# Optimization experiments

Hardware: AMD Instinct MI355X
Metric: run time of the kernel (lower is better)

The kernel has to match this reference:

```python
import jax, jax.numpy as jnp
import numpy as np

NUM_GRAPHS = 1024  # number of graphs in the batch (readout segments)


def setup_inputs() -> dict:
    key = jax.random.key(0)
    ks = jax.random.split(key, 10)
    N, F_IN, F1, F2, E = 100000, 64, 128, 64, 3200000
    x = jax.random.normal(ks[0], (N, F_IN), dtype=jnp.float32)
    adj = jax.random.randint(ks[1], (2, E), 0, N, dtype=jnp.int64)
    batch = jnp.sort(jax.random.randint(ks[2], (N,), 0, NUM_GRAPHS, dtype=jnp.int64))
    def xavier(k, shape):
        fan_in, fan_out = shape
        lim = jnp.sqrt(6.0 / (fan_in + fan_out))
        return jax.random.uniform(k, shape, jnp.float32, -lim, lim)
    W1 = xavier(ks[3], (F_IN, F1)); b1 = jax.random.uniform(ks[4], (F1,), jnp.float32)
    W2 = xavier(ks[5], (F1, F2));  b2 = jax.random.uniform(ks[6], (F2,), jnp.float32)
    Wm = xavier(ks[7], (2 * F2, F2)); bm = jax.random.uniform(ks[8], (F2,), jnp.float32)
    return {"x": x, "adj": adj, "batch": batch,
            "W1": W1, "b1": b1, "W2": W2, "b2": b2, "Wm": Wm, "bm": bm}


def _gcn_conv(x, W, b, src, dst):
    # GCNConv: out = D^{-1/2} (A + I) D^{-1/2} X W + b
    N = x.shape[0]
    h = x @ W  # [N, F_out]
    loops = jnp.arange(N, dtype=src.dtype)
    src_a = jnp.concatenate([src, loops])  # add self-loops
    dst_a = jnp.concatenate([dst, loops])
    deg = jax.ops.segment_sum(jnp.ones(src_a.shape[0], h.dtype), dst_a, num_segments=N)
    dinv = jax.lax.rsqrt(deg)  # deg >= 1 due to self-loops
    norm = dinv[src_a] * dinv[dst_a]  # [E+N]
    msg = h[src_a] * norm[:, None]    # gather + scale (memory-bound)
    return jax.ops.segment_sum(msg, dst_a, num_segments=N) + b


def _readout_meanmax(x, batch):
    G = NUM_GRAPHS
    s = jax.ops.segment_sum(x, batch, num_segments=G)
    cnt = jax.ops.segment_sum(jnp.ones(x.shape[0], x.dtype), batch, num_segments=G)
    mean = s / jnp.maximum(cnt, 1.0)[:, None]
    mx = jax.ops.segment_max(x, batch, num_segments=G)
    return jnp.concatenate([mean, mx], axis=1)  # [G, 2*F2]


def reference(x, adj, batch, W1, b1, W2, b2, Wm, bm):
    src, dst = adj[0], adj[1]
    h = jax.nn.relu(_gcn_conv(x, W1, b1, src, dst))
    h = _gcn_conv(h, W2, b2, src, dst)
    r = _readout_meanmax(h, batch)
    return r @ Wm + bm
```

## Files before the change

### kernel.cpp

```cpp
#include <hip/hip_runtime.h>
#include <hip/hip_fp16.h>
#include <cstdint>
#include <cstddef>

#define NGRAPH 1024
#define CHUNK 8192
#define SCTHREADS 512
#define SCIT (CHUNK / SCTHREADS)
#define MAXB 512
#define CAP 16384

typedef _Float16 f16x8 __attribute__((ext_vector_type(8)));
typedef float f32x4 __attribute__((ext_vector_type(4)));
typedef float f32x2 __attribute__((ext_vector_type(2)));


__global__ __launch_bounds__(SCTHREADS) void scatter1_kernel(const int* __restrict__ src,
        const int* __restrict__ dst, int E, int B,
        int* __restrict__ bcnt, unsigned* __restrict__ ebuck) {
    __shared__ unsigned sorted[CHUNK];
    __shared__ int h[MAXB];
    __shared__ int lo[MAXB];
    __shared__ int cur[MAXB];
    __shared__ int gbase[MAXB];
    int blk = blockIdx.x, tid = threadIdx.x;
    int base = blk * CHUNK;
    int cnt_i = E - base; if (cnt_i > CHUNK) cnt_i = CHUNK;

    h[tid] = 0;
    __syncthreads();

    unsigned rd[SCIT], rs[SCIT];
    #pragma unroll
    for (int it = 0; it < SCIT; ++it) {
        int i = base + tid + it * SCTHREADS;
        if (i < E) {
            rd[it] = (unsigned)dst[i];
            rs[it] = (unsigned)src[i];
            atomicAdd(&h[rd[it] >> 8], 1);
        } else rd[it] = 0xFFFFFFFFu;
    }
    __syncthreads();

    int hv = h[tid];
    if (tid < B) gbase[tid] = hv ? atomicAdd(&bcnt[tid], hv) : 0;

    for (int o = 1; o < SCTHREADS; o <<= 1) {
        int t = (tid >= o) ? h[tid - o] : 0;
        __syncthreads();
        h[tid] += t;
        __syncthreads();
    }
    int excl = h[tid] - hv;
    lo[tid] = excl;
    cur[tid] = excl;
    __syncthreads();

    #pragma unroll
    for (int it = 0; it < SCIT; ++it) {
        if (rd[it] != 0xFFFFFFFFu) {
            int b = rd[it] >> 8;
            int p = atomicAdd(&cur[b], 1);
            sorted[p] = ((rd[it] & 255u) << 24) | rs[it];
        }
    }
    __syncthreads();

    for (int j = tid; j < cnt_i; j += SCTHREADS) {
        int l = (int)(((long long)j * B) / cnt_i);
        if (l > B - 1) l = B - 1;
        while (lo[l] > j) --l;
        while (l + 1 < B && lo[l + 1] <= j) ++l;
        ebuck[(size_t)l * CAP + gbase[l] + (j - lo[l])] = sorted[j];
    }
}

__global__ __launch_bounds__(256) void fine_kernel(const unsigned* __restrict__ ebuck,
        const int* __restrict__ bcnt, const float* __restrict__ x, int N, int B,
        int* __restrict__ row_beg, int* __restrict__ row_end, float* __restrict__ dinv,
        int* __restrict__ esrc, unsigned char* __restrict__ xs) {
    __shared__ int hcnt[256];
    __shared__ int sc[256];
    __shared__ int loff[256];
    __shared__ float sdinv[256];
    int b = blockIdx.x, tid = threadIdx.x;
    int beg = b * CAP;
    int cnt = bcnt[b];
    hcnt[tid] = 0;
    __syncthreads();
    for (int e = tid; e < cnt; e += 256)
        atomicAdd(&hcnt[ebuck[beg + e] >> 24], 1);
    __syncthreads();
    int v = hcnt[tid];
    int n = (b << 8) + tid;
    int vp = (v + 15) & ~15;
    if (vp < 48) vp = 48;
    if (n >= N) vp = 0;
    sc[tid] = vp; __syncthreads();
    for (int o = 1; o < 256; o <<= 1) {
        int t = (tid >= o) ? sc[tid - o] : 0;
        __syncthreads();
        sc[tid] += t;
        __syncthreads();
    }
    int excl = sc[tid] - vp;
    float d = rsqrtf((float)(v + 1));
    if (n < N) {
        row_beg[n] = beg + excl;
        row_end[n] = beg + excl + vp;
        dinv[n] = d;
    }
    loff[tid] = excl;
    sdinv[tid] = d;
    __syncthreads();
    for (int e = tid; e < cnt; e += 256) {
        unsigned u = ebuck[beg + e];
        int p = atomicAdd(&loff[u >> 24], 1);
        esrc[beg + p] = (int)(u & 0xFFFFFF);
    }
    for (int p = excl + v; p < excl + vp; ++p) esrc[beg + p] = N;
    const float4* xr = (const float4*)x;
    #pragma unroll
    for (int it = 0; it < 16; ++it) {
        int j = tid + it * 256;
        int node = j >> 4, cc = j & 15;
        int gn = (b << 8) + node;
        if (gn < N) {
            float dd = sdinv[node];
            float4 vv = xr[(size_t)gn * 16 + cc];
            int lo2 = __builtin_amdgcn_cvt_pk_fp8_f32(vv.x * dd, vv.y * dd, 0, false);
            int hi2 = __builtin_amdgcn_cvt_pk_fp8_f32(vv.z * dd, vv.w * dd, 0, false);
            ((unsigned*)xs)[(size_t)gn * 16 + cc] =
                (unsigned)(lo2 & 0xffff) | ((unsigned)(hi2 & 0xffff) << 16);
        }
    }
}

__global__ __launch_bounds__(256) void prep_kernel(const float* __restrict__ W1,
        const float* __restrict__ W2, __half* __restrict__ W1s, __half* __restrict__ W2s,
        const int* __restrict__ batch, int N, int* __restrict__ goff,
        int* __restrict__ bcnt, unsigned char* __restrict__ xsq,
        unsigned char* __restrict__ tsq, float* __restrict__ zbias) {
    int t = threadIdx.x;
    if (blockIdx.x == 0) {
        #pragma unroll
        for (int it = 0; it < 4; ++it) {
            int s = t + it * 256;
            int n = s & 15, q = (s >> 4) & 3, nt = (s >> 6) & 7, ks = s >> 9;
            int k0 = ks * 32 + q * 8, col = nt * 16 + n;
            __align__(16) __half h[8];
            #pragma unroll
            for (int j = 0; j < 8; ++j) h[j] = (__half)W1[(k0 + j) * 128 + col];
            *((uint4*)&W1s[(size_t)s * 8]) = *(uint4*)h;
        }
        #pragma unroll
        for (int it = 0; it < 4; ++it) {
            int s = t + it * 256;
            int n = s & 15, q = (s >> 4) & 3, n2 = (s >> 6) & 3, ks2 = s >> 8;
            int k0 = ks2 * 32 + q * 8, col = n2 * 16 + n;
            __align__(16) __half h[8];
            #pragma unroll
            for (int j = 0; j < 8; ++j) h[j] = (__half)W2[(k0 + j) * 64 + col];
            *((uint4*)&W2s[(size_t)s * 8]) = *(uint4*)h;
        }
        uint4 z; z.x = 0; z.y = 0; z.z = 0; z.w = 0;
        if (t < 4)
            ((uint4*)(xsq + (size_t)N * 64))[t] = z;
        if (t < 4)
            ((uint4*)(tsq + (size_t)N * 64))[t] = z;
        if (t < 64) zbias[t] = 0.f;
    } else {
        int g = (blockIdx.x - 1) * 256 + t;
        if (g < MAXB) bcnt[g] = 0;
        if (g > NGRAPH) return;
        if (g == NGRAPH) { goff[g] = N; return; }
        int lo = 0, hi = N;
        while (lo < hi) {
            int mid = (lo + hi) >> 1;
            if (batch[mid] < g) lo = mid + 1; else hi = mid;
        }
        goff[g] = lo;
    }
}

__device__ __forceinline__ void acc8q(f32x2* a, const uint2& u) {
    a[0] += __builtin_amdgcn_cvt_pk_f32_fp8(u.x, false);
    a[1] += __builtin_amdgcn_cvt_pk_f32_fp8(u.x, true);
    a[2] += __builtin_amdgcn_cvt_pk_f32_fp8(u.y, false);
    a[3] += __builtin_amdgcn_cvt_pk_f32_fp8(u.y, true);
}

__device__ __forceinline__ void agg_core_q(const uint2* __restrict__ ts2,
        const int* __restrict__ esrc, int beg, int endp, int n, int g, int c,
        float* a) {
    f32x2 h0[4] = {}, h1[4] = {};
    if (g == 0) acc8q(h0, ts2[(size_t)n * 8 + c]);
    int U = (endp - beg) >> 3;
    int e = beg + g;
    if (U == 6) {
        int i0 = esrc[e], i1 = esrc[e + 8], i2 = esrc[e + 16];
        int i3 = esrc[e + 24], i4 = esrc[e + 32], i5 = esrc[e + 40];
        uint2 u0 = ts2[(size_t)i0 * 8 + c];
        uint2 u1 = ts2[(size_t)i1 * 8 + c];
        uint2 u2 = ts2[(size_t)i2 * 8 + c];
        uint2 u3 = ts2[(size_t)i3 * 8 + c];
        uint2 u4 = ts2[(size_t)i4 * 8 + c];
        uint2 u5 = ts2[(size_t)i5 * 8 + c];
        acc8q(h0, u0); acc8q(h1, u1); acc8q(h0, u2); acc8q(h1, u3);
        acc8q(h0, u4); acc8q(h1, u5);
    } else if (U > 0) {
        int i0 = esrc[e], i1 = esrc[e + 8];
        for (int t = (U >> 1) - 1; t > 0; --t) {
            int j0 = esrc[e + 16], j1 = esrc[e + 24];
            acc8q(h0, ts2[(size_t)i0 * 8 + c]);
            acc8q(h1, ts2[(size_t)i1 * 8 + c]);
            i0 = j0; i1 = j1; e += 16;
        }
        acc8q(h0, ts2[(size_t)i0 * 8 + c]);
        acc8q(h1, ts2[(size_t)i1 * 8 + c]);
    }
    #pragma unroll
    for (int i = 0; i < 4; ++i) {
        a[2 * i]     = h0[i].x + h1[i].x;
        a[2 * i + 1] = h0[i].y + h1[i].y;
    }
}

__global__ __launch_bounds__(256) void agg_q2h_kernel(const unsigned char* __restrict__ ts,
        const int* __restrict__ esrc, const int* __restrict__ row_beg,
        const int* __restrict__ row_end, const float* __restrict__ dinv,
        const float* __restrict__ bias, __half* __restrict__ out, int N) {
    int n = blockIdx.x * 4 + (threadIdx.x >> 6);
    if (n >= N) return;
    int lane = threadIdx.x & 63;
    int g = lane >> 3, c = lane & 7;
    const uint2* ts2 = (const uint2*)ts;
    float a[8];
    agg_core_q(ts2, esrc, row_beg[n], row_end[n], n, g, c, a);
    #pragma unroll
    for (int i = 0; i < 8; ++i) {
        a[i] += __shfl_xor(a[i], 8, 64);
        a[i] += __shfl_xor(a[i], 16, 64);
        a[i] += __shfl_xor(a[i], 32, 64);
    }
    if (g == 0) {
        float d = dinv[n];
        float4 bb0 = ((const float4*)bias)[c * 2];
        float4 bb1 = ((const float4*)bias)[c * 2 + 1];
        __align__(16) __half2 h[4];
        h[0] = __floats2half2_rn(a[0] * d + bb0.x, a[1] * d + bb0.y);
        h[1] = __floats2half2_rn(a[2] * d + bb0.z, a[3] * d + bb0.w);
        h[2] = __floats2half2_rn(a[4] * d + bb1.x, a[5] * d + bb1.y);
        h[3] = __floats2half2_rn(a[6] * d + bb1.z, a[7] * d + bb1.w);
        ((uint4*)out)[(size_t)n * 8 + c] = *(uint4*)h;
    }
}

__global__ __launch_bounds__(256) void fusedmlp_kernel(const __half* __restrict__ A,
        const __half* __restrict__ W1s, const __half* __restrict__ W2s,
        const float* __restrict__ b1, const float* __restrict__ dinv,
        unsigned char* __restrict__ T, int N) {
    __shared__ __align__(16) __half h1t[4][16][136];
    int tid = threadIdx.x;
    int w = tid >> 6, lane = tid & 63;
    int n15 = lane & 15, q = lane >> 4;
    int base = blockIdx.x * 64 + w * 16;

    int m = base + n15; if (m >= N) m = N - 1;
    const uint4* Ar = (const uint4*)(A + (size_t)m * 64);
    uint4 ua0 = Ar[q];
    uint4 ua1 = Ar[4 + q];
    f16x8 a10 = *(f16x8*)&ua0;
    f16x8 a11 = *(f16x8*)&ua1;
    const uint4* W1f = (const uint4*)W1s;
    #pragma unroll
    for (int nt = 0; nt < 8; ++nt) {
        f32x4 c = {0.f, 0.f, 0.f, 0.f};
        uint4 ub0 = W1f[(nt * 4 + q) * 16 + n15];
        uint4 ub1 = W1f[((8 + nt) * 4 + q) * 16 + n15];
        c = __builtin_amdgcn_mfma_f32_16x16x32_f16(a10, *(f16x8*)&ub0, c, 0, 0, 0);
        c = __builtin_amdgcn_mfma_f32_16x16x32_f16(a11, *(f16x8*)&ub1, c, 0, 0, 0);
        float bv = b1[nt * 16 + n15];
        #pragma unroll
        for (int rr = 0; rr < 4; ++rr) {
            float hv = fmaxf(c[rr] + bv, 0.f);
            h1t[w][q * 4 + rr][nt * 16 + n15] = (__half)hv;
        }
    }
    __syncthreads();

    f16x8 a2[4];
    #pragma unroll
    for (int ks2 = 0; ks2 < 4; ++ks2)
        a2[ks2] = *(f16x8*)&h1t[w][n15][ks2 * 32 + q * 8];
    const uint4* W2f = (const uint4*)W2s;
    #pragma unroll
    for (int n2 = 0; n2 < 4; ++n2) {
        f32x4 c = {0.f, 0.f, 0.f, 0.f};
        #pragma unroll
        for (int ks2 = 0; ks2 < 4; ++ks2) {
            uint4 ub = W2f[((ks2 * 4 + n2) * 4 + q) * 16 + n15];
            c = __builtin_amdgcn_mfma_f32_16x16x32_f16(a2[ks2], *(f16x8*)&ub, c, 0, 0, 0);
        }
        #pragma unroll
        for (int rr = 0; rr < 4; ++rr) {
            int node = base + q * 4 + rr;
            if (node < N) {
                float v = c[rr] * dinv[node];
                int pk = __builtin_amdgcn_cvt_pk_fp8_f32(v, v, 0, false);
                T[(size_t)node * 64 + n2 * 16 + n15] = (unsigned char)(pk & 0xff);
            }
        }
    }
}

__global__ __launch_bounds__(256) void readout_head_kernel(const __half* __restrict__ h2,
        const int* __restrict__ goff, const float* __restrict__ Wm,
        const float* __restrict__ bm, float* __restrict__ out) {
    int g = blockIdx.x;
    int beg = goff[g], end = goff[g + 1];
    int f = threadIdx.x & 63;
    int c = threadIdx.x >> 6;
    float s = 0.f, m = -3.4e38f;
    for (int n = beg + c; n < end; n += 4) {
        float v = __half2float(h2[(size_t)n * 64 + f]);
        s += v;
        m = fmaxf(m, v);
    }
    __shared__ float ss[4][64], sm[4][64];
    __shared__ float rr[128];
    ss[c][f] = s; sm[c][f] = m;
    __syncthreads();
    if (c == 0) {
        float S = ss[0][f] + ss[1][f] + ss[2][f] + ss[3][f];
        float M = fmaxf(fmaxf(sm[0][f], sm[1][f]), fmaxf(sm[2][f], sm[3][f]));
        int cnt = end - beg;
        rr[f] = (cnt > 0) ? S / (float)cnt : 0.f;
        rr[64 + f] = (cnt > 0) ? M : 0.f;
    }
    __syncthreads();
    if (threadIdx.x < 64) {
        int j = threadIdx.x;
        float acc = bm[j];
        #pragma unroll 4
        for (int k = 0; k < 128; ++k)
            acc = fmaf(rr[k], Wm[k * 64 + j], acc);
        out[(size_t)g * 64 + j] = acc;
    }
}

extern "C" void kernel_launch(void* const* d_in, const int* in_sizes, int n_in,
                              void* d_out, int out_size, void* d_ws, size_t ws_size,
                              hipStream_t stream) {
    const float* x    = (const float*)d_in[0];
    const int*  adj   = (const int*)d_in[1];
    const int*  batch = (const int*)d_in[2];
    const float* W1   = (const float*)d_in[3];
    const float* b1   = (const float*)d_in[4];
    const float* W2   = (const float*)d_in[5];
    const float* b2   = (const float*)d_in[6];
    const float* Wm   = (const float*)d_in[7];
    const float* bm   = (const float*)d_in[8];
    float* out = (float*)d_out;

    const int N = in_sizes[0] / 64;
    const int E = in_sizes[1] / 2;
    const int* src = adj;
    const int* dst = adj + E;
    const int B = (N + 255) >> 8;
    const int nblocks = (E + CHUNK - 1) / CHUNK;

    char* w = (char*)d_ws;
    size_t off = 0;
    auto carve = [&](size_t bytes) -> void* {
        void* p = w + off;
        off += (bytes + 255) & ~(size_t)255;
        return p;
    };
    size_t halfbuf = (size_t)N * 64 * 2;
    float* dinv    = (float*)carve((size_t)N * 4);
    int*   row_beg = (int*)  carve((size_t)N * 4);
    int*   row_end = (int*)  carve((size_t)N * 4);
    int*   esrc    = (int*)  carve((size_t)B * CAP * 4);
    unsigned* ebuck= (unsigned*)carve((size_t)B * CAP * 4);
    int*   bcnt    = (int*)  carve((MAXB + 1) * 4);
    int*   goff    = (int*)  carve((NGRAPH + 1) * 4);
    __half* W1s    = (__half*)carve(8192 * 2);
    __half* W2s    = (__half*)carve(8192 * 2);
    unsigned char* xs_q = (unsigned char*)carve((size_t)N * 64 + 64);
    __half* agg1h  = (__half*)carve(halfbuf);
    __half* h2     = (__half*)carve(halfbuf);
    unsigned char* ts_q = (unsigned char*)carve((size_t)N * 64 + 64);
    float* zbias   = (float*)carve(256);

    prep_kernel<<<1 + (NGRAPH + 256) / 256, 256, 0, stream>>>(W1, W2, W1s, W2s,
                                                              batch, N, goff, bcnt,
                                                              xs_q, ts_q, zbias);

    scatter1_kernel<<<nblocks, SCTHREADS, 0, stream>>>(src, dst, E, B, bcnt, ebuck);
    fine_kernel<<<B, 256, 0, stream>>>(ebuck, bcnt, x, N, B, row_beg, row_end,
                                       dinv, esrc, xs_q);

    agg_q2h_kernel<<<(N + 3) / 4, 256, 0, stream>>>(xs_q, esrc, row_beg, row_end,
                                                    dinv, zbias, agg1h, N);

    fusedmlp_kernel<<<(N + 63) / 64, 256, 0, stream>>>(agg1h, W1s, W2s, b1, dinv, ts_q, N);

    agg_q2h_kernel<<<(N + 3) / 4, 256, 0, stream>>>(ts_q, esrc, row_beg, row_end,
                                                    dinv, b2, h2, N);

    readout_head_kernel<<<NGRAPH, 256, 0, stream>>>(h2, goff, Wm, bm, out);
}
```

Baseline: 286.4 us.

## Widen fine_kernel to 1024 threads and cache bucket edges in registers

The per-bucket fine kernel now runs 1024 threads instead of 256. Each thread keeps up to 12 bucket entries in registers, so the second pass over ebuck does not reload them from global memory. The padding fill is split across four threads per node and the x quantisation loop is spread over the wider block. The aim is more memory-level parallelism in a kernel that has only about 400 blocks. The cost is higher register use, and three of every four threads sit idle during the 256-wide scan.

```diff
diff --git a/kernel.cpp b/kernel.cpp
--- a/kernel.cpp
+++ b/kernel.cpp
@@ -9,6 +9,8 @@
 #define SCIT (CHUNK / SCTHREADS)
 #define MAXB 512
 #define CAP 16384
+#define FTHREADS 1024
+#define FEPT 12
 
 typedef _Float16 f16x8 __attribute__((ext_vector_type(8)));
 typedef float f32x4 __attribute__((ext_vector_type(4)));
@@ -75,7 +77,7 @@
     }
 }
 
-__global__ __launch_bounds__(256) void fine_kernel(const unsigned* __restrict__ ebuck,
+__global__ __launch_bounds__(FTHREADS) void fine_kernel(const unsigned* __restrict__ ebuck,
         const int* __restrict__ bcnt, const float* __restrict__ x, int N, int B,
         int* __restrict__ row_beg, int* __restrict__ row_end, float* __restrict__ dinv,
         int* __restrict__ esrc, unsigned char* __restrict__ xs) {
@@ -86,43 +88,78 @@
     int b = blockIdx.x, tid = threadIdx.x;
     int beg = b * CAP;
     int cnt = bcnt[b];
-    hcnt[tid] = 0;
-    __syncthreads();
-    for (int e = tid; e < cnt; e += 256)
+    if (tid < 256) hcnt[tid] = 0;
+    __syncthreads();
+
+    unsigned re[FEPT];
+    #pragma unroll
+    for (int it = 0; it < FEPT; ++it) {
+        int e = tid + it * FTHREADS;
+        re[it] = (e < cnt) ? ebuck[beg + e] : 0xFFFFFFFFu;
+    }
+    #pragma unroll
+    for (int it = 0; it < FEPT; ++it)
+        if (re[it] != 0xFFFFFFFFu) atomicAdd(&hcnt[re[it] >> 24], 1);
+    for (int e = tid + FEPT * FTHREADS; e < cnt; e += FTHREADS)
         atomicAdd(&hcnt[ebuck[beg + e] >> 24], 1);
     __syncthreads();
-    int v = hcnt[tid];
-    int n = (b << 8) + tid;
-    int vp = (v + 15) & ~15;
-    if (vp < 48) vp = 48;
-    if (n >= N) vp = 0;
-    sc[tid] = vp; __syncthreads();
+
+    int v = 0, vp = 0;
+    int n = (b << 8) + (tid & 255);
+    if (tid < 256) {
+        v = hcnt[tid];
+        vp = (v + 15) & ~15;
+        if (vp < 48) vp = 48;
+        if (n >= N) vp = 0;
+        sc[tid] = vp;
+    }
+    __syncthreads();
     for (int o = 1; o < 256; o <<= 1) {
-        int t = (tid >= o) ? sc[tid - o] : 0;
+        int t = 0;
+        if (tid < 256 && tid >= o) t = sc[tid - o];
         __syncthreads();
-        sc[tid] += t;
+        if (tid < 256) sc[tid] += t;
         __syncthreads();
     }
-    int excl = sc[tid] - vp;
-    float d = rsqrtf((float)(v + 1));
-    if (n < N) {
-        row_beg[n] = beg + excl;
-        row_end[n] = beg + excl + vp;
-        dinv[n] = d;
-    }
-    loff[tid] = excl;
-    sdinv[tid] = d;
-    __syncthreads();
-    for (int e = tid; e < cnt; e += 256) {
+    if (tid < 256) {
+        int excl = sc[tid] - vp;
+        float d = rsqrtf((float)(v + 1));
+        if (n < N) {
+            row_beg[n] = beg + excl;
+            row_end[n] = beg + excl + vp;
+            dinv[n] = d;
+        }
+        loff[tid] = excl;
+        sdinv[tid] = d;
+    }
+    __syncthreads();
+
+    #pragma unroll
+    for (int it = 0; it < FEPT; ++it) {
+        if (re[it] != 0xFFFFFFFFu) {
+            int p = atomicAdd(&loff[re[it] >> 24], 1);
+            esrc[beg + p] = (int)(re[it] & 0xFFFFFF);
+        }
+    }
+    for (int e = tid + FEPT * FTHREADS; e < cnt; e += FTHREADS) {
         unsigned u = ebuck[beg + e];
         int p = atomicAdd(&loff[u >> 24], 1);
         esrc[beg + p] = (int)(u & 0xFFFFFF);
     }
-    for (int p = excl + v; p < excl + vp; ++p) esrc[beg + p] = N;
+
+    {
+        int node = tid & 255, l4 = tid >> 8;
+        int scn = sc[node];
+        int vpn = scn - (node ? sc[node - 1] : 0);
+        int vn = hcnt[node];
+        for (int p = scn - vpn + vn + l4; p < scn; p += 4)
+            esrc[beg + p] = N;
+    }
+
     const float4* xr = (const float4*)x;
     #pragma unroll
-    for (int it = 0; it < 16; ++it) {
-        int j = tid + it * 256;
+    for (int it = 0; it < 4; ++it) {
+        int j = tid + it * FTHREADS;
         int node = j >> 4, cc = j & 15;
         int gn = (b << 8) + node;
         if (gn < N) {
@@ -398,8 +435,8 @@
                                                               xs_q, ts_q, zbias);
 
     scatter1_kernel<<<nblocks, SCTHREADS, 0, stream>>>(src, dst, E, B, bcnt, ebuck);
-    fine_kernel<<<B, 256, 0, stream>>>(ebuck, bcnt, x, N, B, row_beg, row_end,
-                                       dinv, esrc, xs_q);
+    fine_kernel<<<B, FTHREADS, 0, stream>>>(ebuck, bcnt, x, N, B, row_beg, row_end,
+                                            dinv, esrc, xs_q);
 
     agg_q2h_kernel<<<(N + 3) / 4, 256, 0, stream>>>(xs_q, esrc, row_beg, row_end,
                                                     dinv, zbias, agg1h, N);
```

Result: slower. 294.5 us (+2.8%).

## Replace two-pass bucket sort CSR build with global atomic degree count and scatter

Applied to the files above, without the earlier changes.

Replaces the shared-memory bucketed counting sort (scatter1 + fine kernels) with a simpler CSR build: a global atomic degree histogram, a per-block scan to set row offsets, a separate fp8 pack kernel, and a global-atomic scatter of source indices into rows. This removes the intermediate ebuck buffer and one full pass over the edges. The cost is heavy global atomic contention on 100k counters, done twice over 3.2M edges, and nondeterministic edge order within each row.

```diff
diff --git a/kernel.cpp b/kernel.cpp
--- a/kernel.cpp
+++ b/kernel.cpp
@@ -4,142 +4,86 @@
 #include <cstddef>
 
 #define NGRAPH 1024
-#define CHUNK 8192
-#define SCTHREADS 512
-#define SCIT (CHUNK / SCTHREADS)
 #define MAXB 512
 #define CAP 16384
+#define WIDE 2048
 
 typedef _Float16 f16x8 __attribute__((ext_vector_type(8)));
 typedef float f32x4 __attribute__((ext_vector_type(4)));
 typedef float f32x2 __attribute__((ext_vector_type(2)));
 
 
-__global__ __launch_bounds__(SCTHREADS) void scatter1_kernel(const int* __restrict__ src,
-        const int* __restrict__ dst, int E, int B,
-        int* __restrict__ bcnt, unsigned* __restrict__ ebuck) {
-    __shared__ unsigned sorted[CHUNK];
-    __shared__ int h[MAXB];
-    __shared__ int lo[MAXB];
-    __shared__ int cur[MAXB];
-    __shared__ int gbase[MAXB];
-    int blk = blockIdx.x, tid = threadIdx.x;
-    int base = blk * CHUNK;
-    int cnt_i = E - base; if (cnt_i > CHUNK) cnt_i = CHUNK;
-
-    h[tid] = 0;
-    __syncthreads();
-
-    unsigned rd[SCIT], rs[SCIT];
-    #pragma unroll
-    for (int it = 0; it < SCIT; ++it) {
-        int i = base + tid + it * SCTHREADS;
-        if (i < E) {
-            rd[it] = (unsigned)dst[i];
-            rs[it] = (unsigned)src[i];
-            atomicAdd(&h[rd[it] >> 8], 1);
-        } else rd[it] = 0xFFFFFFFFu;
-    }
-    __syncthreads();
-
-    int hv = h[tid];
-    if (tid < B) gbase[tid] = hv ? atomicAdd(&bcnt[tid], hv) : 0;
-
-    for (int o = 1; o < SCTHREADS; o <<= 1) {
-        int t = (tid >= o) ? h[tid - o] : 0;
-        __syncthreads();
-        h[tid] += t;
-        __syncthreads();
-    }
-    int excl = h[tid] - hv;
-    lo[tid] = excl;
-    cur[tid] = excl;
-    __syncthreads();
-
-    #pragma unroll
-    for (int it = 0; it < SCIT; ++it) {
-        if (rd[it] != 0xFFFFFFFFu) {
-            int b = rd[it] >> 8;
-            int p = atomicAdd(&cur[b], 1);
-            sorted[p] = ((rd[it] & 255u) << 24) | rs[it];
-        }
-    }
-    __syncthreads();
-
-    for (int j = tid; j < cnt_i; j += SCTHREADS) {
-        int l = (int)(((long long)j * B) / cnt_i);
-        if (l > B - 1) l = B - 1;
-        while (lo[l] > j) --l;
-        while (l + 1 < B && lo[l + 1] <= j) ++l;
-        ebuck[(size_t)l * CAP + gbase[l] + (j - lo[l])] = sorted[j];
-    }
-}
-
-__global__ __launch_bounds__(256) void fine_kernel(const unsigned* __restrict__ ebuck,
-        const int* __restrict__ bcnt, const float* __restrict__ x, int N, int B,
+__global__ __launch_bounds__(256) void deg_kernel(const int* __restrict__ dst, int E,
+        int* __restrict__ deg) {
+    int i = blockIdx.x * 256 + threadIdx.x;
+    int stride = gridDim.x * 256;
+    for (; i < E; i += stride) atomicAdd(&deg[dst[i]], 1);
+}
+
+__global__ __launch_bounds__(256) void rowb_kernel(const int* __restrict__ deg, int N,
         int* __restrict__ row_beg, int* __restrict__ row_end, float* __restrict__ dinv,
-        int* __restrict__ esrc, unsigned char* __restrict__ xs) {
-    __shared__ int hcnt[256];
+        int* __restrict__ gcur, int* __restrict__ esrc) {
     __shared__ int sc[256];
-    __shared__ int loff[256];
-    __shared__ float sdinv[256];
-    int b = blockIdx.x, tid = threadIdx.x;
+    int b = blockIdx.x, t = threadIdx.x;
     int beg = b * CAP;
-    int cnt = bcnt[b];
-    hcnt[tid] = 0;
-    __syncthreads();
-    for (int e = tid; e < cnt; e += 256)
-        atomicAdd(&hcnt[ebuck[beg + e] >> 24], 1);
-    __syncthreads();
-    int v = hcnt[tid];
-    int n = (b << 8) + tid;
+    int n = (b << 8) + t;
+    int v = (n < N) ? deg[n] : 0;
     int vp = (v + 15) & ~15;
     if (vp < 48) vp = 48;
     if (n >= N) vp = 0;
-    sc[tid] = vp; __syncthreads();
+    sc[t] = vp;
+    __syncthreads();
     for (int o = 1; o < 256; o <<= 1) {
-        int t = (tid >= o) ? sc[tid - o] : 0;
+        int x = (t >= o) ? sc[t - o] : 0;
         __syncthreads();
-        sc[tid] += t;
+        sc[t] += x;
         __syncthreads();
     }
-    int excl = sc[tid] - vp;
-    float d = rsqrtf((float)(v + 1));
+    int excl = sc[t] - vp;
     if (n < N) {
+        float d = rsqrtf((float)(v + 1));
         row_beg[n] = beg + excl;
         row_end[n] = beg + excl + vp;
         dinv[n] = d;
-    }
-    loff[tid] = excl;
-    sdinv[tid] = d;
-    __syncthreads();
-    for (int e = tid; e < cnt; e += 256) {
-        unsigned u = ebuck[beg + e];
-        int p = atomicAdd(&loff[u >> 24], 1);
-        esrc[beg + p] = (int)(u & 0xFFFFFF);
-    }
-    for (int p = excl + v; p < excl + vp; ++p) esrc[beg + p] = N;
+        gcur[n] = beg + excl;
+        for (int p = excl + v; p < excl + vp; ++p)
+            esrc[beg + p] = N;
+    }
+}
+
+__global__ __launch_bounds__(256) void pack_kernel(const float* __restrict__ x,
+        const float* __restrict__ dinv, int N, unsigned char* __restrict__ xs) {
+    int j = blockIdx.x * 256 + threadIdx.x;
+    int total = N * 16;
+    int stride = gridDim.x * 256;
     const float4* xr = (const float4*)x;
-    #pragma unroll
-    for (int it = 0; it < 16; ++it) {
-        int j = tid + it * 256;
+    for (; j < total; j += stride) {
         int node = j >> 4, cc = j & 15;
-        int gn = (b << 8) + node;
-        if (gn < N) {
-            float dd = sdinv[node];
-            float4 vv = xr[(size_t)gn * 16 + cc];
-            int lo2 = __builtin_amdgcn_cvt_pk_fp8_f32(vv.x * dd, vv.y * dd, 0, false);
-            int hi2 = __builtin_amdgcn_cvt_pk_fp8_f32(vv.z * dd, vv.w * dd, 0, false);
-            ((unsigned*)xs)[(size_t)gn * 16 + cc] =
-                (unsigned)(lo2 & 0xffff) | ((unsigned)(hi2 & 0xffff) << 16);
-        }
+        float dd = dinv[node];
+        float4 vv = xr[(size_t)node * 16 + cc];
+        int lo2 = __builtin_amdgcn_cvt_pk_fp8_f32(vv.x * dd, vv.y * dd, 0, false);
+        int hi2 = __builtin_amdgcn_cvt_pk_fp8_f32(vv.z * dd, vv.w * dd, 0, false);
+        ((unsigned*)xs)[(size_t)node * 16 + cc] =
+            (unsigned)(lo2 & 0xffff) | ((unsigned)(hi2 & 0xffff) << 16);
+    }
+}
+
+__global__ __launch_bounds__(256) void scatter_csr_kernel(const int* __restrict__ src,
+        const int* __restrict__ dst, int E, int* __restrict__ gcur,
+        int* __restrict__ esrc) {
+    int i = blockIdx.x * 256 + threadIdx.x;
+    int stride = gridDim.x * 256;
+    for (; i < E; i += stride) {
+        int s = src[i], d = dst[i];
+        int p = atomicAdd(&gcur[d], 1);
+        esrc[p] = s;
     }
 }
 
 __global__ __launch_bounds__(256) void prep_kernel(const float* __restrict__ W1,
         const float* __restrict__ W2, __half* __restrict__ W1s, __half* __restrict__ W2s,
         const int* __restrict__ batch, int N, int* __restrict__ goff,
-        int* __restrict__ bcnt, unsigned char* __restrict__ xsq,
+        int* __restrict__ deg, unsigned char* __restrict__ xsq,
         unsigned char* __restrict__ tsq, float* __restrict__ zbias) {
     int t = threadIdx.x;
     if (blockIdx.x == 0) {
@@ -171,9 +115,9 @@
         if (t < 64) zbias[t] = 0.f;
     } else {
         int g = (blockIdx.x - 1) * 256 + t;
-        if (g < MAXB) bcnt[g] = 0;
+        if (g < N) deg[g] = 0;
+        if (g == NGRAPH) { goff[g] = N; return; }
         if (g > NGRAPH) return;
-        if (g == NGRAPH) { goff[g] = N; return; }
         int lo = 0, hi = N;
         while (lo < hi) {
             int mid = (lo + hi) >> 1;
@@ -368,7 +312,6 @@
     const int* src = adj;
     const int* dst = adj + E;
     const int B = (N + 255) >> 8;
-    const int nblocks = (E + CHUNK - 1) / CHUNK;
 
     char* w = (char*)d_ws;
     size_t off = 0;
@@ -382,8 +325,8 @@
     int*   row_beg = (int*)  carve((size_t)N * 4);
     int*   row_end = (int*)  carve((size_t)N * 4);
     int*   esrc    = (int*)  carve((size_t)B * CAP * 4);
-    unsigned* ebuck= (unsigned*)carve((size_t)B * CAP * 4);
-    int*   bcnt    = (int*)  carve((MAXB + 1) * 4);
+    int*   deg     = (int*)  carve((size_t)N * 4);
+    int*   gcur    = (int*)  carve((size_t)N * 4);
     int*   goff    = (int*)  carve((NGRAPH + 1) * 4);
     __half* W1s    = (__half*)carve(8192 * 2);
     __half* W2s    = (__half*)carve(8192 * 2);
@@ -393,13 +336,14 @@
     unsigned char* ts_q = (unsigned char*)carve((size_t)N * 64 + 64);
     float* zbias   = (float*)carve(256);
 
-    prep_kernel<<<1 + (NGRAPH + 256) / 256, 256, 0, stream>>>(W1, W2, W1s, W2s,
-                                                              batch, N, goff, bcnt,
-                                                              xs_q, ts_q, zbias);
-
-    scatter1_kernel<<<nblocks, SCTHREADS, 0, stream>>>(src, dst, E, B, bcnt, ebuck);
-    fine_kernel<<<B, 256, 0, stream>>>(ebuck, bcnt, x, N, B, row_beg, row_end,
-                                       dinv, esrc, xs_q);
+    int pgrid = 1 + ((N > NGRAPH + 1 ? N : NGRAPH + 1) + 255) / 256;
+    prep_kernel<<<pgrid, 256, 0, stream>>>(W1, W2, W1s, W2s, batch, N, goff,
+                                           deg, xs_q, ts_q, zbias);
+
+    deg_kernel<<<WIDE, 256, 0, stream>>>(dst, E, deg);
+    rowb_kernel<<<B, 256, 0, stream>>>(deg, N, row_beg, row_end, dinv, gcur, esrc);
+    pack_kernel<<<WIDE, 256, 0, stream>>>(x, dinv, N, xs_q);
+    scatter_csr_kernel<<<WIDE, 256, 0, stream>>>(src, dst, E, gcur, esrc);
 
     agg_q2h_kernel<<<(N + 3) / 4, 256, 0, stream>>>(xs_q, esrc, row_beg, row_end,
                                                     dinv, zbias, agg1h, N);
```

After: 645.3 us. 125% more time.
